# Performance work log

Measured on AMD Instinct MI355X. Metric: run time of the kernel, lower is better.

## Reference

```python
import jax, jax.numpy as jnp
import numpy as np

EPS = 1e-06

def _feature_map(x):
    # elu_feature_map: phi(x) = elu(x) + 1  (strictly positive features)
    return jax.nn.elu(x) + 1.0

def setup_inputs() -> dict:
    key = jax.random.key(0)
    kq, kk, kv = jax.random.split(key, 3)
    N, L, H, D, M = 2, 2048, 8, 64, 64
    return {
        "queries": jax.random.normal(kq, (N, L, H, D), dtype=jnp.float32),
        "keys": jax.random.normal(kk, (N, L, H, D), dtype=jnp.float32),
        "values": jax.random.normal(kv, (N, L, H, M), dtype=jnp.float32),
    }

def reference(queries, keys, values):
    Q = _feature_map(queries)   # [N,L,H,D]
    K = _feature_map(keys)      # [N,L,H,D]
    # normalizer: Z_i = 1 / (Q_i . sum_{j<=i} K_j + eps)
    Z = 1.0 / (jnp.einsum('nlhi,nlhi->nlh', Q, jnp.cumsum(K, axis=1)) + EPS)
    # causal linear attention: S_i = sum_{j<=i} K_j outer V_j ; out_i = Q_i @ S_i
    S = jnp.cumsum(jnp.einsum('nlhd,nlhm->nlhdm', K, values), axis=1)  # [N,L,H,D,M]
    V = jnp.einsum('nlhd,nlhdm->nlhm', Q, S)
    return V * Z[:, :, :, None]
```

## Files before the change

kernel.cpp:

```cpp
#include <hip/hip_runtime.h>


namespace {
constexpr int N_ = 2, L_ = 2048, H_ = 8, D_ = 64, M_ = 64;
constexpr int C  = 64;
constexpr int G  = L_ / C;
constexpr int NH = N_ * H_;
constexpr int LDH = H_ * D_;
constexpr int TS  = 72;
constexpr float EPS_ = 1e-6f;
}

typedef __attribute__((ext_vector_type(8))) short short8;
typedef __attribute__((ext_vector_type(4))) float f32x4;

__device__ __forceinline__ float phi(float x) {
    return x > 0.0f ? x + 1.0f : __expf(x);
}
__device__ __forceinline__ unsigned short f2bf(float x) {
    unsigned int u = __float_as_uint(x);
    u += 0x7fffu + ((u >> 16) & 1u);
    return (unsigned short)(u >> 16);
}
__device__ __forceinline__ float bf2f(unsigned short h) {
    return __uint_as_float(((unsigned int)h) << 16);
}

__global__ __launch_bounds__(256, 4) void k_chunksum(
    const float* __restrict__ keys, const float* __restrict__ values,
    unsigned short* __restrict__ wsSb, float* __restrict__ wsK)
{
    __shared__ __align__(16) unsigned short Kt[C * TS];
    __shared__ __align__(16) unsigned short Vt[C * TS];
    const int bid = blockIdx.x;
    const int g = bid % G, nh = bid / G;
    const int n = nh / H_, h = nh % H_;
    const int t = threadIdx.x;
    const size_t base = ((size_t)(n * L_ + g * C) * H_ + h) * D_;

#pragma unroll
    for (int r = 0; r < 4; ++r) {
        const int f = t + 256 * r;
        const int j = f >> 4, c = (f & 15) * 4;
        const size_t ga = base + (size_t)j * LDH + c;
        const float4 kv = *(const float4*)(keys + ga);
        const float4 vv = *(const float4*)(values + ga);
        Kt[(c + 0) * TS + j] = f2bf(phi(kv.x));
        Kt[(c + 1) * TS + j] = f2bf(phi(kv.y));
        Kt[(c + 2) * TS + j] = f2bf(phi(kv.z));
        Kt[(c + 3) * TS + j] = f2bf(phi(kv.w));
        Vt[(c + 0) * TS + j] = f2bf(vv.x);
        Vt[(c + 1) * TS + j] = f2bf(vv.y);
        Vt[(c + 2) * TS + j] = f2bf(vv.z);
        Vt[(c + 3) * TS + j] = f2bf(vv.w);
    }
    __syncthreads();

    const int w = t >> 6, lane = t & 63;
    const int row16 = lane & 15, quad = lane >> 4;

    f32x4 acc[4] = {f32x4{0,0,0,0}, f32x4{0,0,0,0}, f32x4{0,0,0,0}, f32x4{0,0,0,0}};
    f32x4 accK = f32x4{0,0,0,0};
    short8 ones;
#pragma unroll
    for (int i = 0; i < 8; ++i) ones[i] = (short)0x3F80;

#pragma unroll
    for (int kt = 0; kt < 2; ++kt) {
        const short8 a = *(const short8*)&Kt[(16 * w + row16) * TS + quad * 8 + 32 * kt];
#pragma unroll
        for (int c = 0; c < 4; ++c) {
            const short8 b = *(const short8*)&Vt[(16 * c + row16) * TS + quad * 8 + 32 * kt];
            acc[c] = __builtin_amdgcn_mfma_f32_16x16x32_bf16(a, b, acc[c], 0, 0, 0);
        }
        accK = __builtin_amdgcn_mfma_f32_16x16x32_bf16(a, ones, accK, 0, 0, 0);
    }

    unsigned short* Sc = wsSb + (size_t)bid * (D_ * M_);
#pragma unroll
    for (int c = 0; c < 4; ++c) {
        ushort4 pk;
        pk.x = f2bf(acc[c][0]); pk.y = f2bf(acc[c][1]);
        pk.z = f2bf(acc[c][2]); pk.w = f2bf(acc[c][3]);
        *(ushort4*)(Sc + (16 * c + row16) * D_ + 16 * w + quad * 4) = pk;
    }

    if (row16 == 0) {
#pragma unroll
        for (int r = 0; r < 4; ++r)
            wsK[(size_t)bid * D_ + 16 * w + quad * 4 + r] = accK[r];
    }
}

__global__ __launch_bounds__(256) void k_scan(
    unsigned short* __restrict__ wsSb, float* __restrict__ wsK)
{
    const int bid = blockIdx.x;
    const int nh = bid >> 3, q = bid & 7;
    const int t = threadIdx.x;

    unsigned int* base =
        (unsigned int*)(wsSb + (size_t)nh * G * (D_ * M_) + q * 512 + t * 2);
    float r0 = 0.f, r1 = 0.f;
#pragma unroll
    for (int g = 0; g < G; ++g) {
        unsigned int* p = base + (size_t)g * (D_ * M_ / 2);
        const unsigned int v = *p;
        const float v0 = bf2f((unsigned short)(v & 0xffffu));
        const float v1 = bf2f((unsigned short)(v >> 16));
        *p = ((unsigned int)f2bf(r1) << 16) | (unsigned int)f2bf(r0);
        r0 += v0; r1 += v1;
    }

    if (q == 0 && t < D_) {
        float rk = 0.f;
        float* kb = wsK + (size_t)nh * G * D_ + t;
#pragma unroll
        for (int g = 0; g < G; ++g) {
            float* p = kb + (size_t)g * D_;
            const float v = *p;
            *p = rk;
            rk += v;
        }
    }
}

__global__ __launch_bounds__(256, 4) void k_out(
    const float* __restrict__ queries, const float* __restrict__ keys,
    const float* __restrict__ values, float* __restrict__ out,
    const unsigned short* __restrict__ wsSb, const float* __restrict__ wsK)
{
    __shared__ __align__(16) unsigned short Qb[C * TS];
    __shared__ __align__(16) unsigned short Kb[C * TS];
    __shared__ __align__(16) unsigned short Vt[C * TS];
    __shared__ __align__(16) unsigned short St[C * TS];
    __shared__ float Rs[C];
    __shared__ float Zs[C];

    const int bid = blockIdx.x;
    const int g = bid % G, nh = bid / G;
    const int n = nh / H_, h = nh % H_;
    const int t = threadIdx.x;
    const size_t base = ((size_t)(n * L_ + g * C) * H_ + h) * D_;
    const unsigned short* Spb = wsSb + (size_t)bid * (D_ * M_);
    const float* kpref = wsK + (size_t)bid * D_;

#pragma unroll
    for (int r = 0; r < 4; ++r) {
        const int f = t + 256 * r;
        const int row = f >> 4, c = (f & 15) * 4;
        const size_t ga = base + (size_t)row * LDH + c;
        const float4 qv = *(const float4*)(queries + ga);
        const float4 kv = *(const float4*)(keys + ga);
        const float4 vv = *(const float4*)(values + ga);
        Qb[row * TS + c + 0] = f2bf(phi(qv.x));
        Qb[row * TS + c + 1] = f2bf(phi(qv.y));
        Qb[row * TS + c + 2] = f2bf(phi(qv.z));
        Qb[row * TS + c + 3] = f2bf(phi(qv.w));
        Kb[row * TS + c + 0] = f2bf(phi(kv.x));
        Kb[row * TS + c + 1] = f2bf(phi(kv.y));
        Kb[row * TS + c + 2] = f2bf(phi(kv.z));
        Kb[row * TS + c + 3] = f2bf(phi(kv.w));
        Vt[(c + 0) * TS + row] = f2bf(vv.x);
        Vt[(c + 1) * TS + row] = f2bf(vv.y);
        Vt[(c + 2) * TS + row] = f2bf(vv.z);
        Vt[(c + 3) * TS + row] = f2bf(vv.w);
    }
#pragma unroll
    for (int r = 0; r < 2; ++r) {
        const int idx = t + 256 * r;
        const int m = idx >> 3, dg = (idx & 7) * 8;
        *(short8*)&St[m * TS + dg] = *(const short8*)(Spb + m * D_ + dg);
    }
    __syncthreads();

    const int w = t >> 6, lane = t & 63;
    const int row16 = lane & 15, quad = lane >> 4;

    short8 aq[2];
#pragma unroll
    for (int kt = 0; kt < 2; ++kt)
        aq[kt] = *(const short8*)&Qb[(16 * w + row16) * TS + quad * 8 + 32 * kt];

    f32x4 accA[4] = {f32x4{0,0,0,0}, f32x4{0,0,0,0}, f32x4{0,0,0,0}, f32x4{0,0,0,0}};
#pragma unroll
    for (int kt = 0; kt < 2; ++kt)
#pragma unroll
        for (int c = 0; c < 4; ++c) {
            const short8 b = *(const short8*)&Kb[(16 * c + row16) * TS + quad * 8 + 32 * kt];
            accA[c] = __builtin_amdgcn_mfma_f32_16x16x32_bf16(aq[kt], b, accA[c], 0, 0, 0);
        }

    float rs[4] = {0.f, 0.f, 0.f, 0.f};
#pragma unroll
    for (int c = 0; c < 4; ++c)
#pragma unroll
        for (int r = 0; r < 4; ++r) {
            const int row = 16 * w + quad * 4 + r;
            const int col = 16 * c + row16;
            const float v = (col <= row) ? accA[c][r] : 0.f;
            accA[c][r] = v;
            rs[r] += v;
        }
#pragma unroll
    for (int off = 1; off < 16; off <<= 1)
#pragma unroll
        for (int r = 0; r < 4; ++r)
            rs[r] += __shfl_xor(rs[r], off, 64);
    if (row16 == 0) {
#pragma unroll
        for (int r = 0; r < 4; ++r)
            Rs[16 * w + quad * 4 + r] = rs[r];
    }
    __syncthreads();

#pragma unroll
    for (int c = 0; c < 4; ++c)
#pragma unroll
        for (int r = 0; r < 4; ++r)
            Kb[(16 * w + quad * 4 + r) * TS + 16 * c + row16] = f2bf(accA[c][r]);

    if (t < C) {
        float zd = 0.f;
#pragma unroll 8
        for (int d = 0; d < D_; ++d)
            zd += bf2f(Qb[t * TS + d]) * kpref[d];
        Zs[t] = 1.0f / (zd + Rs[t] + EPS_);
    }
    __syncthreads();

    f32x4 accO[4] = {f32x4{0,0,0,0}, f32x4{0,0,0,0}, f32x4{0,0,0,0}, f32x4{0,0,0,0}};
#pragma unroll
    for (int kt = 0; kt < 2; ++kt) {
        const short8 aA = *(const short8*)&Kb[(16 * w + row16) * TS + quad * 8 + 32 * kt];
#pragma unroll
        for (int c = 0; c < 4; ++c) {
            const short8 bV = *(const short8*)&Vt[(16 * c + row16) * TS + quad * 8 + 32 * kt];
            accO[c] = __builtin_amdgcn_mfma_f32_16x16x32_bf16(aA, bV, accO[c], 0, 0, 0);
        }
#pragma unroll
        for (int c = 0; c < 4; ++c) {
            const short8 bS = *(const short8*)&St[(16 * c + row16) * TS + quad * 8 + 32 * kt];
            accO[c] = __builtin_amdgcn_mfma_f32_16x16x32_bf16(aq[kt], bS, accO[c], 0, 0, 0);
        }
    }

#pragma unroll
    for (int r = 0; r < 4; ++r) {
        const int row = 16 * w + quad * 4 + r;
        const float z = Zs[row];
        const size_t ob = ((size_t)(n * L_ + g * C + row) * H_ + h) * M_;
#pragma unroll
        for (int c = 0; c < 4; ++c)
            out[ob + 16 * c + row16] = accO[c][r] * z;
    }
}

extern "C" void kernel_launch(void* const* d_in, const int* in_sizes, int n_in,
                              void* d_out, int out_size, void* d_ws, size_t ws_size,
                              hipStream_t stream) {
    const float* q = (const float*)d_in[0];
    const float* k = (const float*)d_in[1];
    const float* v = (const float*)d_in[2];
    float* out = (float*)d_out;
    unsigned short* wsSb = (unsigned short*)d_ws;
    float* wsK = (float*)((char*)d_ws + (size_t)NH * G * D_ * M_ * 2);

    k_chunksum<<<dim3(NH * G), dim3(256), 0, stream>>>(k, v, wsSb, wsK);
    k_scan<<<dim3(NH * 8), dim3(256), 0, stream>>>(wsSb, wsK);
    k_out<<<dim3(NH * G), dim3(256), 0, stream>>>(q, k, v, out, wsSb, wsK);
}
```

Measured before the change: 84.67 us.

## Fuse chunk-state prefix scan into output kernel, dropping separate scan launch

Removes the k_scan kernel. Each k_out block now sums the chunk states (bf16) and K-sums of all earlier chunks itself, with per-thread register accumulators, and writes the resulting prefix state into shared memory. This removes one kernel launch and the serialized read-modify-write pass over the workspace. The cost is redundant work: late chunks read up to 31 prior chunk states, giving quadratic total global traffic and load imbalance across blocks. The prefix is also now accumulated in fp32 from bf16 inputs instead of from a bf16 running sum.

After: 86.50 us. +2.2%, slower.

```diff
diff --git a/kernel.cpp b/kernel.cpp
--- a/kernel.cpp
+++ b/kernel.cpp
@@ -92,39 +92,6 @@
     }
 }
 
-__global__ __launch_bounds__(256) void k_scan(
-    unsigned short* __restrict__ wsSb, float* __restrict__ wsK)
-{
-    const int bid = blockIdx.x;
-    const int nh = bid >> 3, q = bid & 7;
-    const int t = threadIdx.x;
-
-    unsigned int* base =
-        (unsigned int*)(wsSb + (size_t)nh * G * (D_ * M_) + q * 512 + t * 2);
-    float r0 = 0.f, r1 = 0.f;
-#pragma unroll
-    for (int g = 0; g < G; ++g) {
-        unsigned int* p = base + (size_t)g * (D_ * M_ / 2);
-        const unsigned int v = *p;
-        const float v0 = bf2f((unsigned short)(v & 0xffffu));
-        const float v1 = bf2f((unsigned short)(v >> 16));
-        *p = ((unsigned int)f2bf(r1) << 16) | (unsigned int)f2bf(r0);
-        r0 += v0; r1 += v1;
-    }
-
-    if (q == 0 && t < D_) {
-        float rk = 0.f;
-        float* kb = wsK + (size_t)nh * G * D_ + t;
-#pragma unroll
-        for (int g = 0; g < G; ++g) {
-            float* p = kb + (size_t)g * D_;
-            const float v = *p;
-            *p = rk;
-            rk += v;
-        }
-    }
-}
-
 __global__ __launch_bounds__(256, 4) void k_out(
     const float* __restrict__ queries, const float* __restrict__ keys,
     const float* __restrict__ values, float* __restrict__ out,
@@ -142,8 +109,53 @@
     const int n = nh / H_, h = nh % H_;
     const int t = threadIdx.x;
     const size_t base = ((size_t)(n * L_ + g * C) * H_ + h) * D_;
-    const unsigned short* Spb = wsSb + (size_t)bid * (D_ * M_);
-    const float* kpref = wsK + (size_t)bid * D_;
+
+    float ps[16] = {0.f,0.f,0.f,0.f,0.f,0.f,0.f,0.f,
+                    0.f,0.f,0.f,0.f,0.f,0.f,0.f,0.f};
+    float kp = 0.f;
+    {
+        const unsigned short* Sb = wsSb + (size_t)nh * G * (D_ * M_) + t * 16;
+        const float* Kbase = wsK + (size_t)nh * G * D_ + (t & 63);
+        int gp = 0;
+        for (; gp + 2 <= g; gp += 2) {
+            const uint4 u0 = *(const uint4*)(Sb + (size_t)(gp    ) * (D_ * M_));
+            const uint4 u1 = *(const uint4*)(Sb + (size_t)(gp    ) * (D_ * M_) + 8);
+            const uint4 u2 = *(const uint4*)(Sb + (size_t)(gp + 1) * (D_ * M_));
+            const uint4 u3 = *(const uint4*)(Sb + (size_t)(gp + 1) * (D_ * M_) + 8);
+            const float k0 = Kbase[(size_t)(gp) * D_];
+            const float k1 = Kbase[(size_t)(gp + 1) * D_];
+            const unsigned int w0[4] = {u0.x, u0.y, u0.z, u0.w};
+            const unsigned int w1[4] = {u1.x, u1.y, u1.z, u1.w};
+            const unsigned int w2[4] = {u2.x, u2.y, u2.z, u2.w};
+            const unsigned int w3[4] = {u3.x, u3.y, u3.z, u3.w};
+#pragma unroll
+            for (int i = 0; i < 4; ++i) {
+                ps[2*i]   += bf2f((unsigned short)(w0[i] & 0xffffu))
+                           + bf2f((unsigned short)(w2[i] & 0xffffu));
+                ps[2*i+1] += bf2f((unsigned short)(w0[i] >> 16))
+                           + bf2f((unsigned short)(w2[i] >> 16));
+                ps[8+2*i]   += bf2f((unsigned short)(w1[i] & 0xffffu))
+                             + bf2f((unsigned short)(w3[i] & 0xffffu));
+                ps[8+2*i+1] += bf2f((unsigned short)(w1[i] >> 16))
+                             + bf2f((unsigned short)(w3[i] >> 16));
+            }
+            kp += k0 + k1;
+        }
+        if (gp < g) {
+            const uint4 u0 = *(const uint4*)(Sb + (size_t)gp * (D_ * M_));
+            const uint4 u1 = *(const uint4*)(Sb + (size_t)gp * (D_ * M_) + 8);
+            const unsigned int w0[4] = {u0.x, u0.y, u0.z, u0.w};
+            const unsigned int w1[4] = {u1.x, u1.y, u1.z, u1.w};
+#pragma unroll
+            for (int i = 0; i < 4; ++i) {
+                ps[2*i]     += bf2f((unsigned short)(w0[i] & 0xffffu));
+                ps[2*i+1]   += bf2f((unsigned short)(w0[i] >> 16));
+                ps[8+2*i]   += bf2f((unsigned short)(w1[i] & 0xffffu));
+                ps[8+2*i+1] += bf2f((unsigned short)(w1[i] >> 16));
+            }
+            kp += Kbase[(size_t)gp * D_];
+        }
+    }
 
 #pragma unroll
     for (int r = 0; r < 4; ++r) {
@@ -166,11 +178,13 @@
         Vt[(c + 2) * TS + row] = f2bf(vv.z);
         Vt[(c + 3) * TS + row] = f2bf(vv.w);
     }
-#pragma unroll
-    for (int r = 0; r < 2; ++r) {
-        const int idx = t + 256 * r;
-        const int m = idx >> 3, dg = (idx & 7) * 8;
-        *(short8*)&St[m * TS + dg] = *(const short8*)(Spb + m * D_ + dg);
+    {
+        const int m0s = t >> 2, d0s = (t & 3) * 16;
+        short8 p0, p1;
+#pragma unroll
+        for (int i = 0; i < 8; ++i) { p0[i] = (short)f2bf(ps[i]); p1[i] = (short)f2bf(ps[8 + i]); }
+        *(short8*)&St[m0s * TS + d0s]     = p0;
+        *(short8*)&St[m0s * TS + d0s + 8] = p1;
     }
     __syncthreads();
 
@@ -224,7 +238,7 @@
         float zd = 0.f;
 #pragma unroll 8
         for (int d = 0; d < D_; ++d)
-            zd += bf2f(Qb[t * TS + d]) * kpref[d];
+            zd += bf2f(Qb[t * TS + d]) * __shfl(kp, d, 64);
         Zs[t] = 1.0f / (zd + Rs[t] + EPS_);
     }
     __syncthreads();
@@ -267,6 +281,5 @@
     float* wsK = (float*)((char*)d_ws + (size_t)NH * G * D_ * M_ * 2);
 
     k_chunksum<<<dim3(NH * G), dim3(256), 0, stream>>>(k, v, wsSb, wsK);
-    k_scan<<<dim3(NH * 8), dim3(256), 0, stream>>>(wsSb, wsK);
     k_out<<<dim3(NH * G), dim3(256), 0, stream>>>(q, k, v, out, wsSb, wsK);
 }
```
